# Kernel tuning notes

Measured on AMD Instinct MI355X. Metric: run time of the kernel, lower is better.

The kernel has to match this reference:

```python
import jax, jax.numpy as jnp
import numpy as np

B, HEADS, T, QH, QW, D = 2, 8, 8, 16, 16, 64
KT, KH, KW = T, QH, QW  # key shape == query shape


def _rel_index(q_n, k_n):
    q_ratio = round(max(k_n / q_n, 1.0))
    k_ratio = round(max(q_n / k_n, 1.0))
    d = jnp.arange(q_n)[:, None] * q_ratio - jnp.arange(k_n)[None, :] * k_ratio
    return d + (k_n - 1) * k_ratio  # [q_n, k_n] indices into embedding table


def setup_inputs() -> dict:
    key = jax.random.key(0)
    k1, k2, k3, k4, k5 = jax.random.split(key, 5)
    query = jax.random.normal(k1, (B, HEADS, T * QH * QW, D), dtype=jnp.float32)
    scores = jax.random.normal(k2, (B, HEADS, T * QH * QW, KT * KH * KW), dtype=jnp.float32)
    height_emb = jax.random.normal(k3, (2 * (max(QH, KH) - 1) + 1, D), dtype=jnp.float32)
    width_emb = jax.random.normal(k4, (2 * (max(QW, KW) - 1) + 1, D), dtype=jnp.float32)
    time_emb = jax.random.normal(k5, (2 * (max(T, KT) - 1) + 1, D), dtype=jnp.float32)
    return {"query": query, "scores": scores, "height_emb": height_emb,
            "width_emb": width_emb, "time_emb": time_emb}


def reference(query, scores, height_emb, width_emb, time_emb):
    # gather relative-position embeddings (static indices)
    Rh = height_emb[_rel_index(QH, KH)]   # [qh, kh, D]
    Rw = width_emb[_rel_index(QW, KW)]    # [qw, kw, D]
    Rt = time_emb[_rel_index(T, KT)]      # [t,  kt, D]

    q = query.reshape(B, HEADS, T, QH, QW, D)
    rel_h = jnp.einsum('bNthwc,hkc->bNthwk', q, Rh)  # [B,N,T,qh,qw,kh]
    rel_w = jnp.einsum('bNthwc,wkc->bNthwk', q, Rw)  # [B,N,T,qh,qw,kw]
    rel_t = jnp.einsum('bNthwc,tkc->bNthwk', q, Rt)  # [B,N,T,qh,qw,kt]

    s = scores.reshape(B, HEADS, T, QH, QW, KT, KH, KW)
    s = s + rel_h[:, :, :, :, :, None, :, None]
    s = s + rel_w[:, :, :, :, :, None, None, :]
    s = s + rel_t[:, :, :, :, :, :, None, None]
    return s.reshape(B, HEADS, T * QH * QW, KT * KH * KW)
```

## Files before the change

kernel.cpp:

```cpp
#include <hip/hip_runtime.h>


#define ROWS 4

typedef float v4f __attribute__((ext_vector_type(4)));

__global__ __launch_bounds__(256) void relpos_fused_v3(
    const float* __restrict__ query,
    const float* __restrict__ scores,
    const float* __restrict__ hemb,
    const float* __restrict__ wemb,
    const float* __restrict__ temb,
    float* __restrict__ out)
{
    __shared__ float biasH[ROWS][16];
    __shared__ float biasW[ROWS][16];
    __shared__ float biasT[ROWS][8];

    const int bid  = blockIdx.x;
    const int tid  = threadIdx.x;
    const int wv   = tid >> 6;
    const int lane = tid & 63;

    const int r0   = bid * ROWS;
    const int row  = (r0 + wv) & 2047;
    const int t    = row >> 8;
    const int qh   = (row >> 4) & 15;
    const int qw   = row & 15;

    if (lane < 40) {
        const float* emb;
        int eidx;
        if (lane < 16)      { emb = hemb; eidx = qh - lane + 15; }
        else if (lane < 32) { emb = wemb; eidx = qw - (lane - 16) + 15; }
        else                { emb = temb; eidx = t  - (lane - 32) + 7; }
        const v4f* e4 = (const v4f*)(emb + eidx * 64);
        const v4f* q4 = (const v4f*)(query + (size_t)(r0 + wv) * 64);
        v4f a4 = (v4f)(0.f);
        #pragma unroll
        for (int k = 0; k < 16; ++k) {
            a4 += q4[k] * e4[k];
        }
        const float acc = (a4.x + a4.y) + (a4.z + a4.w);
        if (lane < 16)      biasH[wv][lane] = acc;
        else if (lane < 32) biasW[wv][lane - 16] = acc;
        else                biasT[wv][lane - 32] = acc;
    }
    __syncthreads();

    const size_t base4 = (size_t)bid * (ROWS * 512);
    const v4f* s4p = (const v4f*)scores + base4;
    v4f* o4p = (v4f*)out + base4;

    #pragma unroll
    for (int i = 0; i < 2 * ROWS; ++i) {
        const int idx = tid + i * 256;
        const int rl  = idx >> 9;
        const int j   = idx & 511;
        v4f s = __builtin_nontemporal_load(&s4p[idx]);
        const float a = biasT[rl][j >> 6] + biasH[rl][(j >> 2) & 15];
        const v4f w = ((const v4f*)biasW[rl])[j & 3];
        v4f o = s + a + w;
        __builtin_nontemporal_store(o, &o4p[idx]);
    }
}

extern "C" void kernel_launch(void* const* d_in, const int* in_sizes, int n_in,
                              void* d_out, int out_size, void* d_ws, size_t ws_size,
                              hipStream_t stream) {
    const float* query  = (const float*)d_in[0];
    const float* scores = (const float*)d_in[1];
    const float* hemb   = (const float*)d_in[2];
    const float* wemb   = (const float*)d_in[3];
    const float* temb   = (const float*)d_in[4];
    float* out = (float*)d_out;

    relpos_fused_v3<<<32768 / ROWS, 256, 0, stream>>>(
        query, scores, hemb, wemb, temb, out);
}
```

Baseline: 104.7 us.

## Give each wave its own row, drop block barrier, batch loads upfront

```diff
diff --git a/kernel.cpp b/kernel.cpp
--- a/kernel.cpp
+++ b/kernel.cpp
@@ -5,7 +5,7 @@
 
 typedef float v4f __attribute__((ext_vector_type(4)));
 
-__global__ __launch_bounds__(256) void relpos_fused_v3(
+__global__ __launch_bounds__(256, 8) void relpos_fused_v4(
     const float* __restrict__ query,
     const float* __restrict__ scores,
     const float* __restrict__ hemb,
@@ -17,14 +17,13 @@
     __shared__ float biasW[ROWS][16];
     __shared__ float biasT[ROWS][8];
 
-    const int bid  = blockIdx.x;
     const int tid  = threadIdx.x;
     const int wv   = tid >> 6;
     const int lane = tid & 63;
 
-    const int r0   = bid * ROWS;
-    const int row  = (r0 + wv) & 2047;
-    const int t    = row >> 8;
+    const int grow = blockIdx.x * ROWS + wv;
+    const int row  = grow & 2047;
+    const int tt   = row >> 8;
     const int qh   = (row >> 4) & 15;
     const int qw   = row & 15;
 
@@ -33,9 +32,9 @@
         int eidx;
         if (lane < 16)      { emb = hemb; eidx = qh - lane + 15; }
         else if (lane < 32) { emb = wemb; eidx = qw - (lane - 16) + 15; }
-        else                { emb = temb; eidx = t  - (lane - 32) + 7; }
+        else                { emb = temb; eidx = tt - (lane - 32) + 7; }
         const v4f* e4 = (const v4f*)(emb + eidx * 64);
-        const v4f* q4 = (const v4f*)(query + (size_t)(r0 + wv) * 64);
+        const v4f* q4 = (const v4f*)(query + (size_t)grow * 64);
         v4f a4 = (v4f)(0.f);
         #pragma unroll
         for (int k = 0; k < 16; ++k) {
@@ -46,22 +45,25 @@
         else if (lane < 32) biasW[wv][lane - 16] = acc;
         else                biasT[wv][lane - 32] = acc;
     }
-    __syncthreads();
 
-    const size_t base4 = (size_t)bid * (ROWS * 512);
-    const v4f* s4p = (const v4f*)scores + base4;
-    v4f* o4p = (v4f*)out + base4;
+    const float h  = biasH[wv][(lane >> 2) & 15];
+    const v4f  w4  = ((const v4f*)biasW[wv])[lane & 3];
+    const v4f  hw4 = w4 + h;
+    float tv[8];
+    #pragma unroll
+    for (int i = 0; i < 8; ++i) tv[i] = biasT[wv][i];
 
+    const v4f* s4p = (const v4f*)scores + (size_t)grow * 512 + lane;
+    v4f*       o4p = (v4f*)out          + (size_t)grow * 512 + lane;
+
+    v4f s[8];
     #pragma unroll
-    for (int i = 0; i < 2 * ROWS; ++i) {
-        const int idx = tid + i * 256;
-        const int rl  = idx >> 9;
-        const int j   = idx & 511;
-        v4f s = __builtin_nontemporal_load(&s4p[idx]);
-        const float a = biasT[rl][j >> 6] + biasH[rl][(j >> 2) & 15];
-        const v4f w = ((const v4f*)biasW[rl])[j & 3];
-        v4f o = s + a + w;
-        __builtin_nontemporal_store(o, &o4p[idx]);
+    for (int i = 0; i < 8; ++i)
+        s[i] = __builtin_nontemporal_load(&s4p[i * 64]);
+    #pragma unroll
+    for (int i = 0; i < 8; ++i) {
+        v4f o = s[i] + hw4 + tv[i];
+        __builtin_nontemporal_store(o, &o4p[i * 64]);
     }
 }
 
@@ -75,6 +77,6 @@
     const float* temb   = (const float*)d_in[4];
     float* out = (float*)d_out;
 
-    relpos_fused_v3<<<32768 / ROWS, 256, 0, stream>>>(
+    relpos_fused_v4<<<32768 / ROWS, 256, 0, stream>>>(
         query, scores, hemb, wemb, temb, out);
 }
```

Measured after the change: 105.2 us. No clear change (+0.5%).
